# Performance work log

Hardware: AMD Instinct MI355X
Metric: run time of the kernel (lower is better)

## Reference

```python
import jax, jax.numpy as jnp
import numpy as np

NUM_HEADS = 8
EPS = 1e-9


def setup_inputs() -> dict:
    key = jax.random.key(0)
    ks = jax.random.split(key, 8)
    B, N, D = 2, 2048, 512
    s = 1.0 / np.sqrt(D)
    x = jax.random.normal(ks[0], (B, N, D), dtype=jnp.float32)
    adjacency = jax.random.uniform(ks[1], (B, N, N), dtype=jnp.float32)
    # Linear weights stored as (in, out) so application is x @ W + b
    W_q = jax.random.normal(ks[2], (D, D), dtype=jnp.float32) * s
    W_k = jax.random.normal(ks[3], (D, D), dtype=jnp.float32) * s
    W_v = jax.random.normal(ks[4], (D, D), dtype=jnp.float32) * s
    b_q = jnp.zeros((D,), jnp.float32)
    b_k = jnp.zeros((D,), jnp.float32)
    b_v = jnp.zeros((D,), jnp.float32)
    # soul_gate: Linear(2D -> 1); weight stored as flat (2D,), bias scalar
    w_g = jax.random.normal(ks[5], (2 * D,), dtype=jnp.float32) * (1.0 / np.sqrt(2 * D))
    b_g = jnp.zeros((), jnp.float32)
    return {"x": x, "adjacency": adjacency, "W_q": W_q, "b_q": b_q,
            "W_k": W_k, "b_k": b_k, "W_v": W_v, "b_v": b_v,
            "w_g": w_g, "b_g": b_g}


def reference(x, adjacency, W_q, b_q, W_k, b_k, W_v, b_v, w_g, b_g):
    B, N, D = x.shape
    H = NUM_HEADS
    hd = D // H
    Q = (x @ W_q + b_q).reshape(B, N, H, hd)
    K = (x @ W_k + b_k).reshape(B, N, H, hd)
    V = (x @ W_v + b_v).reshape(B, N, H, hd)
    scores = jnp.einsum('bihd,bjhd->bhij', Q, K) / jnp.sqrt(jnp.float32(hd))
    # soul_gate(cat[x_i, x_j]) is linear, so it decomposes exactly:
    # bias[b,i,j] = x[b,i]@w_g[:D] + x[b,j]@w_g[D:] + b_g  (same math, no (B,N,N,2D) tensor)
    a = x @ w_g[:D]          # (B, N) contribution of x_i
    c = x @ w_g[D:]          # (B, N) contribution of x_j
    soul_bias = a[:, :, None] + c[:, None, :] + b_g   # (B, N, N)
    scores = scores + (soul_bias + jnp.log(adjacency + EPS))[:, None, :, :]
    attn = jax.nn.softmax(scores, axis=-1)            # (B, H, N, N)
    out = jnp.einsum('bhij,bjhd->bihd', attn, V).reshape(B, N, D)
    return out + x
```

## Files before the change

kernel.cpp:

```cpp
#include <hip/hip_runtime.h>
#include <hip/hip_bf16.h>

typedef __bf16 bf16x8 __attribute__((ext_vector_type(8)));
typedef float f32x4 __attribute__((ext_vector_type(4)));
typedef unsigned short u16x8 __attribute__((ext_vector_type(8)));

#define LOG2E 1.44269504f

__device__ __forceinline__ unsigned short f2bu(float f) {
    __hip_bfloat16 h = __float2bfloat16(f);
    unsigned short u;
    __builtin_memcpy(&u, &h, 2);
    return u;
}

__device__ __forceinline__ float fexp2(float x) {
#if __has_builtin(__builtin_amdgcn_exp2f)
    return __builtin_amdgcn_exp2f(x);
#else
    return __expf(x * 0.69314718f);
#endif
}

__device__ __forceinline__ float bu2f(unsigned short u) {
    unsigned int v = ((unsigned int)u) << 16;
    float f;
    __builtin_memcpy(&f, &v, 4);
    return f;
}

#define GLDS16(gp, lp) __builtin_amdgcn_global_load_lds( \
    (const __attribute__((address_space(1))) unsigned int*)(gp), \
    (__attribute__((address_space(3))) unsigned int*)(lp), 16, 0, 0)

#define OFF_QS  0u
#define OFF_KB  4194304u
#define OFF_VT  8388608u
#define OFF_CV  12582912u
#define OFF_XB  12599296u
#define OFF_WT  16793600u
#define OFF_MQ  18366464u
#define OFF_PO  35143680u
#define OFF_PL  43532288u

__global__ void k_prepwt(const float* __restrict__ x, const float* __restrict__ wg,
                         const float* __restrict__ w0, const float* __restrict__ w1,
                         const float* __restrict__ w2,
                         unsigned short* __restrict__ xb, float* __restrict__ cv2,
                         unsigned short* __restrict__ wt) {
    if (blockIdx.x < 1024) {
        int row = blockIdx.x * 4 + (threadIdx.x >> 6);
        int l = threadIdx.x & 63;
        const float4* xr = reinterpret_cast<const float4*>(x + (size_t)row * 512);
        float4 a = xr[l * 2], b2 = xr[l * 2 + 1];
        ushort4 o0, o1;
        o0.x = f2bu(a.x);  o0.y = f2bu(a.y);  o0.z = f2bu(a.z);  o0.w = f2bu(a.w);
        o1.x = f2bu(b2.x); o1.y = f2bu(b2.y); o1.z = f2bu(b2.z); o1.w = f2bu(b2.w);
        ushort4* dst = reinterpret_cast<ushort4*>(xb + (size_t)row * 512);
        dst[l * 2] = o0; dst[l * 2 + 1] = o1;
        const float4* wr = reinterpret_cast<const float4*>(wg + 512);
        float4 g0 = wr[l * 2], g1 = wr[l * 2 + 1];
        float s = a.x * g0.x + a.y * g0.y + a.z * g0.z + a.w * g0.w
                + b2.x * g1.x + b2.y * g1.y + b2.z * g1.z + b2.w * g1.w;
#pragma unroll
        for (int off = 32; off >= 1; off >>= 1) s += __shfl_xor(s, off, 64);
        if (l == 0) cv2[row] = fexp2((s - 8.0f) * LOG2E);
    } else {
        int bid2 = blockIdx.x - 1024;
        int z = bid2 >> 6, yy = bid2 & 63;
        int k0 = (yy >> 3) * 64, n0 = (yy & 7) * 64;
        const float* W = (z == 0) ? w0 : ((z == 1) ? w1 : w2);
        __shared__ float T[64][65];
        int c = threadIdx.x & 63, r0 = threadIdx.x >> 6;
#pragma unroll
        for (int i = 0; i < 16; i++) { int r = r0 + i * 4; T[r][c] = W[(k0 + r) * 512 + n0 + c]; }
        __syncthreads();
        unsigned short* Wt = wt + z * (512 * 512);
#pragma unroll
        for (int i = 0; i < 16; i++) { int a = r0 + i * 4; Wt[(n0 + a) * 512 + k0 + c] = f2bu(T[c][a]); }
    }
}

__global__ __launch_bounds__(256) void k_mid(
    const float* __restrict__ adj, const float* __restrict__ cv2,
    unsigned short* __restrict__ mq,
    const unsigned short* __restrict__ xb, const unsigned short* __restrict__ wt,
    const float* __restrict__ bq, const float* __restrict__ bk, const float* __restrict__ bv,
    unsigned short* __restrict__ Qs, unsigned short* __restrict__ Kb,
    unsigned short* __restrict__ Vt) {
    if (blockIdx.x < 8192) {
        int blk = blockIdx.x;
        int bic = blk >> 5, jt = blk & 31;
        int b = bic >> 7, ic = bic & 127;
        int t = threadIdx.x;
        int l = t >> 2, mt = t & 3, q = l >> 4, cl = l & 15;
        int j0 = jt * 64 + 16 * mt + q * 4;
        const float4 av = *reinterpret_cast<const float4*>(
            adj + ((size_t)(b * 2048 + ic * 16 + cl)) * 2048 + j0);
        const float4 cv = *reinterpret_cast<const float4*>(cv2 + b * 2048 + j0);
        ushort4 o;
        o.x = f2bu((av.x + 1e-9f) * cv.x);
        o.y = f2bu((av.y + 1e-9f) * cv.y);
        o.z = f2bu((av.z + 1e-9f) * cv.z);
        o.w = f2bu((av.w + 1e-9f) * cv.w);
        *reinterpret_cast<ushort4*>(mq + (size_t)bic * 32768 + jt * 1024 + l * 16 + mt * 4) = o;
        return;
    }
    int gid = blockIdx.x - 8192;
    int bx = gid & 63, by = (gid >> 6) & 3, z = gid >> 8;
    __shared__ __align__(16) unsigned short As[64 * 32];
    __shared__ __align__(16) unsigned short Bs[128 * 32];
    const unsigned short* Wt = wt + z * (512 * 512);
    const float* bias = (z == 0) ? bq : ((z == 1) ? bk : bv);
    float scale = (z == 0) ? (0.125f * LOG2E) : 1.0f;
    int m0 = bx * 64, n0 = by * 128;
    int tid = threadIdx.x, w = tid >> 6, l = tid & 63;
    int q = l >> 4, cl = l & 15;
    f32x4 acc[8];
#pragma unroll
    for (int nt = 0; nt < 8; nt++)
#pragma unroll
        for (int r = 0; r < 4; r++) acc[nt][r] = 0.f;
    int arow = l >> 2, ach = (l & 3) * 8;
    for (int k0 = 0; k0 < 512; k0 += 32) {
        GLDS16(xb + (size_t)(m0 + w * 16 + arow) * 512 + k0 + ach, As + w * 512);
#pragma unroll
        for (int e = 0; e < 2; e++)
            GLDS16(Wt + (size_t)(n0 + w * 32 + e * 16 + arow) * 512 + k0 + ach, Bs + w * 1024 + e * 512);
        __syncthreads();
        bf16x8 af = *reinterpret_cast<const bf16x8*>(As + (w * 16 + cl) * 32 + q * 8);
#pragma unroll
        for (int nt = 0; nt < 8; nt++) {
            bf16x8 bf = *reinterpret_cast<const bf16x8*>(Bs + (nt * 16 + cl) * 32 + q * 8);
            acc[nt] = __builtin_amdgcn_mfma_f32_16x16x32_bf16(af, bf, acc[nt], 0, 0, 0);
        }
        __syncthreads();
    }
    if (z == 2) {
        int n_ = (m0 + w * 16 + q * 4) & 2047;
        int b_ = (m0 + w * 16) >> 11;
#pragma unroll
        for (int nt = 0; nt < 8; nt++) {
            int col = n0 + nt * 16 + cl;
            int h_ = col >> 6, d_ = col & 63;
            float bv_ = bias[col];
            ushort4 o;
            o.x = f2bu(acc[nt][0] + bv_); o.y = f2bu(acc[nt][1] + bv_);
            o.z = f2bu(acc[nt][2] + bv_); o.w = f2bu(acc[nt][3] + bv_);
            *reinterpret_cast<ushort4*>(Vt + ((size_t)((b_ * 8 + h_) * 64 + d_)) * 2048 + n_) = o;
        }
    } else {
        unsigned short* Cout = (z == 0) ? Qs : Kb;
#pragma unroll
        for (int nt = 0; nt < 8; nt++) {
            int col = n0 + nt * 16 + cl;
            float bv_ = bias[col];
#pragma unroll
            for (int r = 0; r < 4; r++) {
                int row = m0 + w * 16 + q * 4 + r;
                Cout[(size_t)row * 512 + col] = f2bu((acc[nt][r] + bv_) * scale);
            }
        }
    }
}

__global__ __launch_bounds__(256, 2) void k_attn(
    const unsigned short* __restrict__ Qs, const unsigned short* __restrict__ Kb,
    const unsigned short* __restrict__ Vt, const unsigned short* __restrict__ mq,
    unsigned short* __restrict__ PO, float* __restrict__ PL) {
    __shared__ __align__(16) unsigned short Ks[2][4096];
    __shared__ __align__(16) unsigned short Vs[2][4096];
    __shared__ __align__(16) unsigned short PA[4][16 * 72];
    int bid = blockIdx.x;
    int h = bid >> 6, s = bid & 63, b = s >> 5, ig = (s >> 1) & 15, js = s & 1;
    int tid = threadIdx.x, w = tid >> 6, l = tid & 63, q = l >> 4, cl = l & 15;
    int bh = b * 8 + h;
    int ic0 = ig * 8 + w * 2;

    bf16x8 qf[2][2];
#pragma unroll
    for (int rc = 0; rc < 2; rc++) {
        const unsigned short* qp = Qs + (size_t)(b * 2048 + ig * 128 + w * 32 + rc * 16 + cl) * 512 + h * 64 + q * 8;
        qf[rc][0] = *reinterpret_cast<const bf16x8*>(qp);
        qf[rc][1] = *reinterpret_cast<const bf16x8*>(qp + 32);
    }
    bf16x8 ones;
#pragma unroll
    for (int i = 0; i < 8; i++) { unsigned short o1 = 0x3F80; __builtin_memcpy(((unsigned short*)&ones) + i, &o1, 2); }

    f32x4 O[2][4];
    f32x4 Osum[2];
#pragma unroll
    for (int rc = 0; rc < 2; rc++) {
#pragma unroll
        for (int nt = 0; nt < 4; nt++)
#pragma unroll
            for (int r = 0; r < 4; r++) O[rc][nt][r] = 0.f;
#pragma unroll
        for (int r = 0; r < 4; r++) Osum[rc][r] = 0.f;
    }

    const unsigned short* Kh = Kb + (size_t)b * 2048 * 512 + h * 64;
    const unsigned short* Vh = Vt + ((size_t)bh * 64) * 2048;
    const unsigned short* mb0 = mq + (size_t)(b * 128 + ic0) * 32768 + l * 16 + (size_t)(js * 16) * 1024;
    const unsigned short* mb1 = mb0 + 32768;
    unsigned short* pw = &PA[w][0];
    int lrow = l >> 2, lch = (l & 3) * 8;
    int jb0 = js * 1024;

    {
        int jb = jb0;
#pragma unroll
        for (int e = 0; e < 2; e++) {
            int c = w * 2 + e, kk = c >> 2, r16 = (c & 3) * 16;
            GLDS16(Kh + (size_t)(jb + r16 + lrow) * 512 + kk * 32 + lch, &Ks[0][kk * 2048 + r16 * 32]);
            GLDS16(Vh + (size_t)(r16 + lrow) * 2048 + jb + kk * 32 + lch, &Vs[0][kk * 2048 + r16 * 32]);
        }
    }
    u16x8 mn[2][2];
    mn[0][0] = *reinterpret_cast<const u16x8*>(mb0);
    mn[0][1] = *reinterpret_cast<const u16x8*>(mb0 + 8);
    mn[1][0] = *reinterpret_cast<const u16x8*>(mb1);
    mn[1][1] = *reinterpret_cast<const u16x8*>(mb1 + 8);

    for (int t = 0; t < 16; t++) {
        int bufi = t & 1;
        __syncthreads();
        if (t < 15) {
            int jb = jb0 + (t + 1) * 64;
#pragma unroll
            for (int e = 0; e < 2; e++) {
                int c = w * 2 + e, kk = c >> 2, r16 = (c & 3) * 16;
                GLDS16(Kh + (size_t)(jb + r16 + lrow) * 512 + kk * 32 + lch, &Ks[bufi ^ 1][kk * 2048 + r16 * 32]);
                GLDS16(Vh + (size_t)(r16 + lrow) * 2048 + jb + kk * 32 + lch, &Vs[bufi ^ 1][kk * 2048 + r16 * 32]);
            }
        }
        u16x8 mc[2][2];
        mc[0][0] = mn[0][0]; mc[0][1] = mn[0][1]; mc[1][0] = mn[1][0]; mc[1][1] = mn[1][1];
        if (t < 15) {
            size_t off = (size_t)(t + 1) * 1024;
            mn[0][0] = *reinterpret_cast<const u16x8*>(mb0 + off);
            mn[0][1] = *reinterpret_cast<const u16x8*>(mb0 + off + 8);
            mn[1][0] = *reinterpret_cast<const u16x8*>(mb1 + off);
            mn[1][1] = *reinterpret_cast<const u16x8*>(mb1 + off + 8);
        }
        bf16x8 vf[2][4];
#pragma unroll
        for (int jc = 0; jc < 2; jc++)
#pragma unroll
            for (int nt = 0; nt < 4; nt++)
                vf[jc][nt] = *reinterpret_cast<const bf16x8*>(&Vs[bufi][jc * 2048 + (16 * nt + cl) * 32 + q * 8]);
        f32x4 S[2][4];
#pragma unroll
        for (int rc = 0; rc < 2; rc++)
#pragma unroll
            for (int mt = 0; mt < 4; mt++)
#pragma unroll
                for (int r = 0; r < 4; r++) S[rc][mt][r] = 0.f;
#pragma unroll
        for (int mt = 0; mt < 4; mt++) {
            bf16x8 kf0 = *reinterpret_cast<const bf16x8*>(&Ks[bufi][(16 * mt + cl) * 32 + q * 8]);
            bf16x8 kf1 = *reinterpret_cast<const bf16x8*>(&Ks[bufi][2048 + (16 * mt + cl) * 32 + q * 8]);
#pragma unroll
            for (int rc = 0; rc < 2; rc++) {
                S[rc][mt] = __builtin_amdgcn_mfma_f32_16x16x32_bf16(kf0, qf[rc][0], S[rc][mt], 0, 0, 0);
                S[rc][mt] = __builtin_amdgcn_mfma_f32_16x16x32_bf16(kf1, qf[rc][1], S[rc][mt], 0, 0, 0);
            }
        }
#pragma unroll
        for (int rc = 0; rc < 2; rc++) {
#pragma unroll
            for (int mt = 0; mt < 4; mt++) {
                float p0 = fexp2(S[rc][mt][0]) * bu2f((mt < 2) ? mc[rc][0][mt * 4 + 0] : mc[rc][1][(mt - 2) * 4 + 0]);
                float p1 = fexp2(S[rc][mt][1]) * bu2f((mt < 2) ? mc[rc][0][mt * 4 + 1] : mc[rc][1][(mt - 2) * 4 + 1]);
                float p2 = fexp2(S[rc][mt][2]) * bu2f((mt < 2) ? mc[rc][0][mt * 4 + 2] : mc[rc][1][(mt - 2) * 4 + 2]);
                float p3 = fexp2(S[rc][mt][3]) * bu2f((mt < 2) ? mc[rc][0][mt * 4 + 3] : mc[rc][1][(mt - 2) * 4 + 3]);
                ushort4 o;
                o.x = f2bu(p0); o.y = f2bu(p1); o.z = f2bu(p2); o.w = f2bu(p3);
                *reinterpret_cast<ushort4*>(pw + cl * 72 + 16 * mt + q * 4) = o;
            }
#pragma unroll
            for (int jc = 0; jc < 2; jc++) {
                bf16x8 pf = *reinterpret_cast<const bf16x8*>(pw + cl * 72 + jc * 32 + q * 8);
#pragma unroll
                for (int nt = 0; nt < 4; nt++)
                    O[rc][nt] = __builtin_amdgcn_mfma_f32_16x16x32_bf16(pf, vf[jc][nt], O[rc][nt], 0, 0, 0);
                Osum[rc] = __builtin_amdgcn_mfma_f32_16x16x32_bf16(pf, ones, Osum[rc], 0, 0, 0);
            }
        }
    }

#pragma unroll
    for (int rc = 0; rc < 2; rc++) {
        size_t chunk = ((size_t)(bh * 128 + ic0 + rc)) * 2 + js;
        unsigned short* po = PO + chunk * 1024 + l * 16;
#pragma unroll
        for (int r = 0; r < 4; r++) {
            ushort4 o;
            o.x = f2bu(O[rc][0][r]); o.y = f2bu(O[rc][1][r]);
            o.z = f2bu(O[rc][2][r]); o.w = f2bu(O[rc][3][r]);
            *reinterpret_cast<ushort4*>(po + r * 4) = o;
        }
        if (cl == 0) {
#pragma unroll
            for (int r = 0; r < 4; r++)
                PL[chunk * 16 + q * 4 + r] = Osum[rc][r];
        }
    }
}

__global__ void k_comb(const unsigned short* __restrict__ PO, const float* __restrict__ PL,
                       const float* __restrict__ x, float* __restrict__ out) {
    int blk = blockIdx.x;
    int t64 = blk & 31, bh = blk >> 5;
    int b = bh >> 3, h = bh & 7;
    int t = threadIdx.x;
    int l = t >> 2, r = t & 3, q = l >> 4, cl = l & 15;
#pragma unroll
    for (int w = 0; w < 4; w++) {
        int ic = t64 * 4 + w;
        size_t c0 = ((size_t)(bh * 128 + ic)) * 2;
        ushort4 a = *reinterpret_cast<const ushort4*>(PO + c0 * 1024 + t * 4);
        ushort4 c = *reinterpret_cast<const ushort4*>(PO + (c0 + 1) * 1024 + t * 4);
        float inv = 1.0f / (PL[c0 * 16 + q * 4 + r] + PL[c0 * 16 + 16 + q * 4 + r]);
        size_t gro = (size_t)(b * 2048 + ic * 16 + q * 4 + r) * 512 + h * 64;
        out[gro + 0 * 16 + cl] = (bu2f(a.x) + bu2f(c.x)) * inv + x[gro + 0 * 16 + cl];
        out[gro + 1 * 16 + cl] = (bu2f(a.y) + bu2f(c.y)) * inv + x[gro + 1 * 16 + cl];
        out[gro + 2 * 16 + cl] = (bu2f(a.z) + bu2f(c.z)) * inv + x[gro + 2 * 16 + cl];
        out[gro + 3 * 16 + cl] = (bu2f(a.w) + bu2f(c.w)) * inv + x[gro + 3 * 16 + cl];
    }
}

extern "C" void kernel_launch(void* const* d_in, const int* in_sizes, int n_in,
                              void* d_out, int out_size, void* d_ws, size_t ws_size,
                              hipStream_t stream) {
    const float* x   = (const float*)d_in[0];
    const float* adj = (const float*)d_in[1];
    const float* Wq  = (const float*)d_in[2];
    const float* bq  = (const float*)d_in[3];
    const float* Wk  = (const float*)d_in[4];
    const float* bk  = (const float*)d_in[5];
    const float* Wv  = (const float*)d_in[6];
    const float* bv  = (const float*)d_in[7];
    const float* wg  = (const float*)d_in[8];
    float* out = (float*)d_out;
    char* ws = (char*)d_ws;
    unsigned short* Qs = (unsigned short*)(ws + OFF_QS);
    unsigned short* Kb = (unsigned short*)(ws + OFF_KB);
    unsigned short* Vt = (unsigned short*)(ws + OFF_VT);
    float* cv2 = (float*)(ws + OFF_CV);
    unsigned short* xb = (unsigned short*)(ws + OFF_XB);
    unsigned short* wt = (unsigned short*)(ws + OFF_WT);
    unsigned short* mqp = (unsigned short*)(ws + OFF_MQ);
    unsigned short* PO = (unsigned short*)(ws + OFF_PO);
    float* PL = (float*)(ws + OFF_PL);

    k_prepwt<<<1216, 256, 0, stream>>>(x, wg, Wq, Wk, Wv, xb, cv2, wt);
    k_mid<<<8960, 256, 0, stream>>>(adj, cv2, mqp, xb, wt, bq, bk, bv, Qs, Kb, Vt);
    k_attn<<<512, 256, 0, stream>>>(Qs, Kb, Vt, mqp, PO, PL);
    k_comb<<<512, 256, 0, stream>>>(PO, PL, x, out);
}
```

Before: 159.1 us.

## Split attention key range four ways and restructure PV loop for occupancy

```diff
diff --git a/kernel.cpp b/kernel.cpp
--- a/kernel.cpp
+++ b/kernel.cpp
@@ -41,7 +41,7 @@
 #define OFF_WT  16793600u
 #define OFF_MQ  18366464u
 #define OFF_PO  35143680u
-#define OFF_PL  43532288u
+#define OFF_PL  51920896u
 
 __global__ void k_prepwt(const float* __restrict__ x, const float* __restrict__ wg,
                          const float* __restrict__ w0, const float* __restrict__ w1,
@@ -164,15 +164,15 @@
     }
 }
 
-__global__ __launch_bounds__(256, 2) void k_attn(
+__global__ __launch_bounds__(256, 3) void k_attn(
     const unsigned short* __restrict__ Qs, const unsigned short* __restrict__ Kb,
     const unsigned short* __restrict__ Vt, const unsigned short* __restrict__ mq,
     unsigned short* __restrict__ PO, float* __restrict__ PL) {
     __shared__ __align__(16) unsigned short Ks[2][4096];
     __shared__ __align__(16) unsigned short Vs[2][4096];
-    __shared__ __align__(16) unsigned short PA[4][16 * 72];
+    __shared__ __align__(16) unsigned short PA[4][32 * 72];
     int bid = blockIdx.x;
-    int h = bid >> 6, s = bid & 63, b = s >> 5, ig = (s >> 1) & 15, js = s & 1;
+    int h = bid >> 7, b = (bid >> 6) & 1, ig = (bid >> 2) & 15, js = bid & 3;
     int tid = threadIdx.x, w = tid >> 6, l = tid & 63, q = l >> 4, cl = l & 15;
     int bh = b * 8 + h;
     int ic0 = ig * 8 + w * 2;
@@ -202,31 +202,23 @@
 
     const unsigned short* Kh = Kb + (size_t)b * 2048 * 512 + h * 64;
     const unsigned short* Vh = Vt + ((size_t)bh * 64) * 2048;
-    const unsigned short* mb0 = mq + (size_t)(b * 128 + ic0) * 32768 + l * 16 + (size_t)(js * 16) * 1024;
+    const unsigned short* mb0 = mq + (size_t)(b * 128 + ic0) * 32768 + l * 16 + (size_t)(js * 8) * 1024;
     const unsigned short* mb1 = mb0 + 32768;
     unsigned short* pw = &PA[w][0];
     int lrow = l >> 2, lch = (l & 3) * 8;
-    int jb0 = js * 1024;
-
-    {
-        int jb = jb0;
-#pragma unroll
-        for (int e = 0; e < 2; e++) {
-            int c = w * 2 + e, kk = c >> 2, r16 = (c & 3) * 16;
-            GLDS16(Kh + (size_t)(jb + r16 + lrow) * 512 + kk * 32 + lch, &Ks[0][kk * 2048 + r16 * 32]);
-            GLDS16(Vh + (size_t)(r16 + lrow) * 2048 + jb + kk * 32 + lch, &Vs[0][kk * 2048 + r16 * 32]);
-        }
-    }
-    u16x8 mn[2][2];
-    mn[0][0] = *reinterpret_cast<const u16x8*>(mb0);
-    mn[0][1] = *reinterpret_cast<const u16x8*>(mb0 + 8);
-    mn[1][0] = *reinterpret_cast<const u16x8*>(mb1);
-    mn[1][1] = *reinterpret_cast<const u16x8*>(mb1 + 8);
-
-    for (int t = 0; t < 16; t++) {
+    int jb0 = js * 512;
+
+#pragma unroll
+    for (int e = 0; e < 2; e++) {
+        int c = w * 2 + e, kk = c >> 2, r16 = (c & 3) * 16;
+        GLDS16(Kh + (size_t)(jb0 + r16 + lrow) * 512 + kk * 32 + lch, &Ks[0][kk * 2048 + r16 * 32]);
+        GLDS16(Vh + (size_t)(r16 + lrow) * 2048 + jb0 + kk * 32 + lch, &Vs[0][kk * 2048 + r16 * 32]);
+    }
+
+    for (int t = 0; t < 8; t++) {
         int bufi = t & 1;
         __syncthreads();
-        if (t < 15) {
+        if (t < 7) {
             int jb = jb0 + (t + 1) * 64;
 #pragma unroll
             for (int e = 0; e < 2; e++) {
@@ -236,20 +228,13 @@
             }
         }
         u16x8 mc[2][2];
-        mc[0][0] = mn[0][0]; mc[0][1] = mn[0][1]; mc[1][0] = mn[1][0]; mc[1][1] = mn[1][1];
-        if (t < 15) {
-            size_t off = (size_t)(t + 1) * 1024;
-            mn[0][0] = *reinterpret_cast<const u16x8*>(mb0 + off);
-            mn[0][1] = *reinterpret_cast<const u16x8*>(mb0 + off + 8);
-            mn[1][0] = *reinterpret_cast<const u16x8*>(mb1 + off);
-            mn[1][1] = *reinterpret_cast<const u16x8*>(mb1 + off + 8);
-        }
-        bf16x8 vf[2][4];
-#pragma unroll
-        for (int jc = 0; jc < 2; jc++)
-#pragma unroll
-            for (int nt = 0; nt < 4; nt++)
-                vf[jc][nt] = *reinterpret_cast<const bf16x8*>(&Vs[bufi][jc * 2048 + (16 * nt + cl) * 32 + q * 8]);
+        {
+            size_t off = (size_t)t * 1024;
+            mc[0][0] = *reinterpret_cast<const u16x8*>(mb0 + off);
+            mc[0][1] = *reinterpret_cast<const u16x8*>(mb0 + off + 8);
+            mc[1][0] = *reinterpret_cast<const u16x8*>(mb1 + off);
+            mc[1][1] = *reinterpret_cast<const u16x8*>(mb1 + off + 8);
+        }
         f32x4 S[2][4];
 #pragma unroll
         for (int rc = 0; rc < 2; rc++)
@@ -277,22 +262,27 @@
                 float p3 = fexp2(S[rc][mt][3]) * bu2f((mt < 2) ? mc[rc][0][mt * 4 + 3] : mc[rc][1][(mt - 2) * 4 + 3]);
                 ushort4 o;
                 o.x = f2bu(p0); o.y = f2bu(p1); o.z = f2bu(p2); o.w = f2bu(p3);
-                *reinterpret_cast<ushort4*>(pw + cl * 72 + 16 * mt + q * 4) = o;
-            }
-#pragma unroll
-            for (int jc = 0; jc < 2; jc++) {
-                bf16x8 pf = *reinterpret_cast<const bf16x8*>(pw + cl * 72 + jc * 32 + q * 8);
-#pragma unroll
-                for (int nt = 0; nt < 4; nt++)
-                    O[rc][nt] = __builtin_amdgcn_mfma_f32_16x16x32_bf16(pf, vf[jc][nt], O[rc][nt], 0, 0, 0);
-                Osum[rc] = __builtin_amdgcn_mfma_f32_16x16x32_bf16(pf, ones, Osum[rc], 0, 0, 0);
-            }
+                *reinterpret_cast<ushort4*>(pw + rc * (16 * 72) + cl * 72 + 16 * mt + q * 4) = o;
+            }
+        }
+#pragma unroll
+        for (int jc = 0; jc < 2; jc++) {
+            bf16x8 pf0 = *reinterpret_cast<const bf16x8*>(pw + cl * 72 + jc * 32 + q * 8);
+            bf16x8 pf1 = *reinterpret_cast<const bf16x8*>(pw + 16 * 72 + cl * 72 + jc * 32 + q * 8);
+#pragma unroll
+            for (int nt = 0; nt < 4; nt++) {
+                bf16x8 vf = *reinterpret_cast<const bf16x8*>(&Vs[bufi][jc * 2048 + (16 * nt + cl) * 32 + q * 8]);
+                O[0][nt] = __builtin_amdgcn_mfma_f32_16x16x32_bf16(pf0, vf, O[0][nt], 0, 0, 0);
+                O[1][nt] = __builtin_amdgcn_mfma_f32_16x16x32_bf16(pf1, vf, O[1][nt], 0, 0, 0);
+            }
+            Osum[0] = __builtin_amdgcn_mfma_f32_16x16x32_bf16(pf0, ones, Osum[0], 0, 0, 0);
+            Osum[1] = __builtin_amdgcn_mfma_f32_16x16x32_bf16(pf1, ones, Osum[1], 0, 0, 0);
         }
     }
 
 #pragma unroll
     for (int rc = 0; rc < 2; rc++) {
-        size_t chunk = ((size_t)(bh * 128 + ic0 + rc)) * 2 + js;
+        size_t chunk = ((size_t)(bh * 128 + ic0 + rc)) * 4 + js;
         unsigned short* po = PO + chunk * 1024 + l * 16;
 #pragma unroll
         for (int r = 0; r < 4; r++) {
@@ -319,15 +309,20 @@
 #pragma unroll
     for (int w = 0; w < 4; w++) {
         int ic = t64 * 4 + w;
-        size_t c0 = ((size_t)(bh * 128 + ic)) * 2;
-        ushort4 a = *reinterpret_cast<const ushort4*>(PO + c0 * 1024 + t * 4);
-        ushort4 c = *reinterpret_cast<const ushort4*>(PO + (c0 + 1) * 1024 + t * 4);
-        float inv = 1.0f / (PL[c0 * 16 + q * 4 + r] + PL[c0 * 16 + 16 + q * 4 + r]);
+        size_t c0 = ((size_t)(bh * 128 + ic)) * 4;
+        float o0 = 0.f, o1 = 0.f, o2 = 0.f, o3 = 0.f, lsum = 0.f;
+#pragma unroll
+        for (int js = 0; js < 4; js++) {
+            ushort4 a = *reinterpret_cast<const ushort4*>(PO + (c0 + js) * 1024 + t * 4);
+            o0 += bu2f(a.x); o1 += bu2f(a.y); o2 += bu2f(a.z); o3 += bu2f(a.w);
+            lsum += PL[(c0 + js) * 16 + q * 4 + r];
+        }
+        float inv = 1.0f / lsum;
         size_t gro = (size_t)(b * 2048 + ic * 16 + q * 4 + r) * 512 + h * 64;
-        out[gro + 0 * 16 + cl] = (bu2f(a.x) + bu2f(c.x)) * inv + x[gro + 0 * 16 + cl];
-        out[gro + 1 * 16 + cl] = (bu2f(a.y) + bu2f(c.y)) * inv + x[gro + 1 * 16 + cl];
-        out[gro + 2 * 16 + cl] = (bu2f(a.z) + bu2f(c.z)) * inv + x[gro + 2 * 16 + cl];
-        out[gro + 3 * 16 + cl] = (bu2f(a.w) + bu2f(c.w)) * inv + x[gro + 3 * 16 + cl];
+        out[gro + 0 * 16 + cl] = o0 * inv + x[gro + 0 * 16 + cl];
+        out[gro + 1 * 16 + cl] = o1 * inv + x[gro + 1 * 16 + cl];
+        out[gro + 2 * 16 + cl] = o2 * inv + x[gro + 2 * 16 + cl];
+        out[gro + 3 * 16 + cl] = o3 * inv + x[gro + 3 * 16 + cl];
     }
 }
 
@@ -357,6 +352,6 @@
 
     k_prepwt<<<1216, 256, 0, stream>>>(x, wg, Wq, Wk, Wv, xb, cv2, wt);
     k_mid<<<8960, 256, 0, stream>>>(adj, cv2, mqp, xb, wt, bq, bk, bv, Qs, Kb, Vt);
-    k_attn<<<512, 256, 0, stream>>>(Qs, Kb, Vt, mqp, PO, PL);
+    k_attn<<<1024, 256, 0, stream>>>(Qs, Kb, Vt, mqp, PO, PL);
     k_comb<<<512, 256, 0, stream>>>(PO, PL, x, out);
 }
```

After: 156.5 us. No clear change (-1.7%).
